# Kernel optimization log

Hardware: AMD Instinct MI355X
Metric: run time of the kernel (lower is better)

## Reference

```python
import jax, jax.numpy as jnp
import numpy as np

B, N, M = 8, 1024, 1024
D_MODEL, D_HEAD, M_BITS = 1024, 128, 32
SCALE = 1.0 / np.sqrt(M_BITS)


def setup_inputs() -> dict:
    key = jax.random.key(0)
    ks = jax.random.split(key, 11)
    w_std = 1.0 / np.sqrt(D_MODEL)  # ~ nn.Linear init scale
    f32 = jnp.float32
    return {
        "Q": jax.random.normal(ks[0], (B, N, D_MODEL), dtype=f32),
        "K": jax.random.normal(ks[1], (B, M, D_MODEL), dtype=f32),
        "V": jax.random.normal(ks[2], (B, M, D_MODEL), dtype=f32),
        "Wq_boolean": jax.random.normal(ks[3], (D_MODEL, M_BITS), dtype=f32) * w_std,
        "Wk_boolean": jax.random.normal(ks[4], (D_MODEL, M_BITS), dtype=f32) * w_std,
        "Wq_tropical": jax.random.normal(ks[5], (D_MODEL, M_BITS), dtype=f32) * w_std,
        "Wk_tropical": jax.random.normal(ks[6], (D_MODEL, M_BITS), dtype=f32) * w_std,
        "Wq_real": jax.random.normal(ks[7], (D_MODEL, M_BITS), dtype=f32) * w_std,
        "Wk_real": jax.random.normal(ks[8], (D_MODEL, M_BITS), dtype=f32) * w_std,
        "Wv": jax.random.normal(ks[9], (D_MODEL, D_HEAD), dtype=f32) * w_std,
        "fusion_weights": jnp.ones((3,), dtype=f32),
        "mask": jnp.ones((B, N, M), dtype=jnp.int32),
    }


def _tropical_sim(Qe, Ke):
    # max-plus (tropical) witness similarity: sim[b,n,m] = max_d (Qe[b,n,d] + Ke[b,m,d])
    # loop over the small fixed bit dim (M_BITS=32) to avoid a [B,N,M,M_BITS] tensor
    acc = Qe[:, :, 0][:, :, None] + Ke[:, :, 0][:, None, :]
    for b in range(1, M_BITS):
        acc = jnp.maximum(acc, Qe[:, :, b][:, :, None] + Ke[:, :, b][:, None, :])
    return acc  # [B,N,M]


def reference(Q, K, V, Wq_boolean, Wk_boolean, Wq_tropical, Wk_tropical,
              Wq_real, Wk_real, Wv, fusion_weights, mask):
    # --- boolean monoid: hard-binarized codes, bit-match count ---
    Qb = (Q @ Wq_boolean > 0).astype(Q.dtype)   # [B,N,m]
    Kb = (K @ Wk_boolean > 0).astype(K.dtype)   # [B,M,m]
    sim_bool = (jnp.einsum('bnd,bmd->bnm', Qb, Kb)
                + jnp.einsum('bnd,bmd->bnm', 1.0 - Qb, 1.0 - Kb))
    # --- tropical monoid: max-plus over continuous codes ---
    sim_trop = _tropical_sim(Q @ Wq_tropical, K @ Wk_tropical)
    # --- real monoid: inner product of continuous codes ---
    sim_real = jnp.einsum('bnd,bmd->bnm', Q @ Wq_real, K @ Wk_real)
    # --- learned fusion + scaled softmax attention ---
    w = jax.nn.softmax(fusion_weights)
    scores = (w[0] * sim_bool + w[1] * sim_trop + w[2] * sim_real) * SCALE
    scores = jnp.where(mask == 0, -jnp.inf, scores)
    attn = jax.nn.softmax(scores, axis=-1)     # [B,N,M]  (dropout: eval mode, identity)
    out = jnp.einsum('bnm,bmh->bnh', attn, V @ Wv)  # [B,N,d_head]
    return out, attn
```

## Files before the change

kernel.cpp:

```cpp
#include <hip/hip_runtime.h>
#include <hip/hip_fp16.h>
#include <stdint.h>
#include <math.h>


#define SCALE_F 0.17677669529663687f

typedef float4 f4;
typedef unsigned int uint_t;
typedef unsigned short ushort_t;
typedef __attribute__((ext_vector_type(8))) short s16x8;
typedef __attribute__((ext_vector_type(8))) unsigned short u16x8;
typedef __attribute__((ext_vector_type(4))) float f32x4;

__device__ __forceinline__ ushort_t f2bf(float x) {
    unsigned u = __float_as_uint(x);
    return (ushort_t)((u + 0x7FFFu + ((u >> 16) & 1u)) >> 16);
}
__device__ __forceinline__ float bf2f(ushort_t h) {
    return __uint_as_float(((unsigned)h) << 16);
}
__device__ __forceinline__ float f4c(const f4 v, int i) {
    return i == 0 ? v.x : (i == 1 ? v.y : (i == 2 ? v.z : v.w));
}
__device__ __forceinline__ unsigned pk_add(unsigned a, unsigned b) {
    unsigned r;
    asm("v_pk_add_f16 %0, %1, %2" : "=v"(r) : "v"(a), "v"(b));
    return r;
}
__device__ __forceinline__ unsigned pk_max(unsigned a, unsigned b) {
    unsigned r;
    asm("v_pk_max_f16 %0, %1, %2" : "=v"(r) : "v"(a), "v"(b));
    return r;
}
__device__ __forceinline__ float h2f(ushort_t u) {
    __half h;
    *reinterpret_cast<ushort_t*>(&h) = u;
    return __half2float(h);
}
__device__ __forceinline__ ushort_t f2h(float x) {
    __half h = __float2half(x);
    return *reinterpret_cast<ushort_t*>(&h);
}

#define MFMA16(a, b, c) __builtin_amdgcn_mfma_f32_16x16x32_bf16((a), (b), (c), 0, 0, 0)

__device__ __forceinline__ int bo(int col, int kq) {
    return col * 64 + 8 * (kq ^ (col & 7));
}
__device__ __forceinline__ int fillk(int s) {
    return 8 * ((s & 7) ^ ((s >> 3) & 7));
}

__global__ __launch_bounds__(256)
void conv_w_kernel(const float* __restrict__ Wqb, const float* __restrict__ Wkb,
                   const float* __restrict__ Wqt, const float* __restrict__ Wkt,
                   const float* __restrict__ Wqr, const float* __restrict__ Wkr,
                   const float* __restrict__ Wv,
                   ushort_t* __restrict__ Wh, ushort_t* __restrict__ Wm,
                   ushort_t* __restrict__ Wl3,
                   ushort_t* __restrict__ Wvh, ushort_t* __restrict__ Wvm) {
    __shared__ float T[256][33];
    const int t = threadIdx.x;
    const int bid = blockIdx.x;
    const float* src;
    int kb, outRowBase, srcStride, srcColBase, side = 0;
    bool isQK, isBool;
    if (bid < 24) {
        side = bid / 12;
        int cb = (bid % 12) / 4;
        kb = bid & 3;
        const float* mats[6] = {Wqb, Wqt, Wqr, Wkb, Wkt, Wkr};
        src = mats[side * 3 + cb];
        srcStride = 32; srcColBase = 0;
        outRowBase = side * 96 + cb * 32;
        isQK = true; isBool = (cb == 0);
    } else {
        int v = bid - 24;
        int hb = v >> 2; kb = v & 3;
        src = Wv; srcStride = 128; srcColBase = hb * 32;
        outRowBase = hb * 32;
        isQK = false; isBool = false;
    }
    #pragma unroll
    for (int i = 0; i < 8; ++i) {
        int idx = t + i * 256;
        int r = idx >> 3, c4 = idx & 7;
        f4 v = *(const f4*)&src[(size_t)(kb * 256 + r) * srcStride + srcColBase + c4 * 4];
        T[r][c4 * 4 + 0] = v.x; T[r][c4 * 4 + 1] = v.y;
        T[r][c4 * 4 + 2] = v.z; T[r][c4 * 4 + 3] = v.w;
    }
    __syncthreads();
    const int col = t >> 3, kseg = t & 7;
    ushort_t* dh = isQK ? Wh : Wvh;
    ushort_t* dm = isQK ? Wm : Wvm;
    size_t obase = (size_t)(outRowBase + col) * 1024 + kb * 256 + kseg * 32;
    u16x8 ph[4], pm[4], pl[4];
    #pragma unroll
    for (int i = 0; i < 32; ++i) {
        float x = T[kseg * 32 + i][col];
        ushort_t hb_ = f2bf(x);
        float r1 = x - bf2f(hb_);
        ushort_t mb_ = f2bf(r1);
        float r2 = r1 - bf2f(mb_);
        ph[i >> 3][i & 7] = hb_;
        pm[i >> 3][i & 7] = mb_;
        pl[i >> 3][i & 7] = f2bf(r2);
    }
    #pragma unroll
    for (int i = 0; i < 4; ++i) {
        *(u16x8*)&dh[obase + i * 8] = ph[i];
        *(u16x8*)&dm[obase + i * 8] = pm[i];
    }
    if (isBool) {
        size_t lbase = (size_t)(side * 32 + col) * 1024 + kb * 256 + kseg * 32;
        #pragma unroll
        for (int i = 0; i < 4; ++i) *(u16x8*)&Wl3[lbase + i * 8] = pl[i];
    }
}


__global__ __launch_bounds__(256)
void proj_qk_kernel(const float* __restrict__ Q, const float* __restrict__ K,
                    const ushort_t* __restrict__ Wh, const ushort_t* __restrict__ Wm,
                    ushort_t* __restrict__ Qt_q, ushort_t* __restrict__ Kt_q,
                    ushort_t* __restrict__ Qrh, ushort_t* __restrict__ Qrm,
                    ushort_t* __restrict__ Krh, ushort_t* __restrict__ Krm,
                    uint_t* __restrict__ Qbits, uint_t* __restrict__ Kbits) {
    __shared__ ushort_t BH[2][6144];
    __shared__ ushort_t BM[2][4096];
    __shared__ uint_t sb[32];
    const int t = threadIdx.x, lane = t & 63, w = t >> 6;
    const int g = lane >> 4, l15 = lane & 15;
    const int side = blockIdx.x >> 8;
    const int tile = blockIdx.x & 255;
    const int row0 = tile * 32;
    const int rg = w >> 1;
    const int ch = w & 1;
    const float* __restrict__ X = side ? K : Q;
    const float* __restrict__ Xrow = X + (size_t)(row0 + rg * 16 + l15) * 1024;
    if (t < 32) sb[t] = 0;

    const ushort_t* srcH[3]; int dstH[3];
    #pragma unroll
    for (int i = 0; i < 3; ++i) {
        int s = t + i * 256;
        int col = s >> 3;
        srcH[i] = Wh + (size_t)(side * 96 + col) * 1024 + fillk(s);
        dstH[i] = s * 8;
    }
    const ushort_t* srcM[2]; int dstM[2];
    #pragma unroll
    for (int i = 0; i < 2; ++i) {
        int s = t + i * 256;
        int col = s >> 3;
        int f = (col < 32) ? col : col + 32;
        srcM[i] = Wm + (size_t)(side * 96 + f) * 1024 + fillk(s);
        dstM[i] = s * 8;
    }

    f32x4 accB[2], accT[2], accR[2];
    #pragma unroll
    for (int i = 0; i < 2; ++i) {
        accB[i] = f32x4{0.f, 0.f, 0.f, 0.f};
        accT[i] = f32x4{0.f, 0.f, 0.f, 0.f};
        accR[i] = f32x4{0.f, 0.f, 0.f, 0.f};
    }

    f4 arE[4], arO[4];
    u16x8 hE[3], mE[2], hO[3], mO[2];

    auto STAGE_A = [&](int k0, f4* ar) {
        ar[0] = *(const f4*)&Xrow[k0 + g * 8];
        ar[1] = *(const f4*)&Xrow[k0 + g * 8 + 4];
        ar[2] = *(const f4*)&Xrow[k0 + 32 + g * 8];
        ar[3] = *(const f4*)&Xrow[k0 + 32 + g * 8 + 4];
    };
    auto STAGE_B = [&](int k0, u16x8* hh, u16x8* mm) {
        #pragma unroll
        for (int i = 0; i < 3; ++i) hh[i] = *(const u16x8*)(srcH[i] + k0);
        #pragma unroll
        for (int i = 0; i < 2; ++i) mm[i] = *(const u16x8*)(srcM[i] + k0);
    };
    auto WRITE_B = [&](int buf, u16x8* hh, u16x8* mm) {
        #pragma unroll
        for (int i = 0; i < 3; ++i) *(u16x8*)&BH[buf][dstH[i]] = hh[i];
        #pragma unroll
        for (int i = 0; i < 2; ++i) *(u16x8*)&BM[buf][dstM[i]] = mm[i];
    };
    auto COMPUTE = [&](int buf, f4* ar) {
        #pragma unroll
        for (int ks = 0; ks < 2; ++ks) {
            u16x8 ah, am, al;
            #pragma unroll
            for (int j = 0; j < 8; ++j) {
                float x = (j < 4) ? f4c(ar[2 * ks], j) : f4c(ar[2 * ks + 1], j - 4);
                ushort_t hb_ = f2bf(x);
                float r1 = x - bf2f(hb_);
                ushort_t mb_ = f2bf(r1);
                ah[j] = hb_; am[j] = mb_;
                al[j] = f2bf(r1 - bf2f(mb_));
            }
            s16x8 a1 = (s16x8)ah, a2 = (s16x8)am;
            const int kq = ks * 4 + g;
            if (ch == 0) {
                s16x8 a3 = (s16x8)al;
                #pragma unroll
                for (int cf = 0; cf < 2; ++cf) {
                    int col = cf * 16 + l15;
                    s16x8 bh = *(const s16x8*)&BH[buf][bo(col, kq)];
                    s16x8 bm = *(const s16x8*)&BM[buf][bo(col, kq)];
                    accB[cf] = MFMA16(a1, bh, accB[cf]);
                    accB[cf] = MFMA16(a1, bm, accB[cf]);
                    accB[cf] = MFMA16(a2, bh, accB[cf]);
                    accB[cf] = MFMA16(a2, bm, accB[cf]);
                    accB[cf] = MFMA16(a3, bh, accB[cf]);
                }
            } else {
                #pragma unroll
                for (int cf = 0; cf < 2; ++cf) {
                    int col = 32 + cf * 16 + l15;
                    s16x8 bh = *(const s16x8*)&BH[buf][bo(col, kq)];
                    accT[cf] = MFMA16(a1, bh, accT[cf]);
                }
                #pragma unroll
                for (int cf = 0; cf < 2; ++cf) {
                    int colh = 64 + cf * 16 + l15;
                    int colm = 32 + cf * 16 + l15;
                    s16x8 bh = *(const s16x8*)&BH[buf][bo(colh, kq)];
                    s16x8 bm = *(const s16x8*)&BM[buf][bo(colm, kq)];
                    accR[cf] = MFMA16(a1, bh, accR[cf]);
                    accR[cf] = MFMA16(a1, bm, accR[cf]);
                    accR[cf] = MFMA16(a2, bh, accR[cf]);
                }
            }
        }
    };

    STAGE_A(0, arE);
    STAGE_B(0, hE, mE);
    WRITE_B(0, hE, mE);
    __syncthreads();
    for (int cc = 0; cc < 8; ++cc) {
        const int kE = cc * 128;
        STAGE_A(kE + 64, arO);
        STAGE_B(kE + 64, hO, mO);
        COMPUTE(0, arE);
        WRITE_B(1, hO, mO);
        __syncthreads();
        if (cc < 7) {
            STAGE_A(kE + 128, arE);
            STAGE_B(kE + 128, hE, mE);
        }
        COMPUTE(1, arO);
        if (cc < 7) WRITE_B(0, hE, mE);
        __syncthreads();
    }

    if (ch == 0) {
        #pragma unroll
        for (int cf = 0; cf < 2; ++cf)
            #pragma unroll
            for (int r = 0; r < 4; ++r) {
                unsigned long long bm = __ballot(accB[cf][r] > 0.f);
                if (lane == 0) {
                    #pragma unroll
                    for (int gg = 0; gg < 4; ++gg)
                        sb[rg * 16 + gg * 4 + r] |=
                            (uint_t)((bm >> (16 * gg)) & 0xFFFFull) << (16 * cf);
                }
            }
    } else {
        ushort_t* Tt = side ? Kt_q : Qt_q;
        ushort_t* Rh = side ? Krh : Qrh;
        ushort_t* Rm = side ? Krm : Qrm;
        #pragma unroll
        for (int cf = 0; cf < 2; ++cf)
            #pragma unroll
            for (int r = 0; r < 4; ++r) {
                int grow = row0 + rg * 16 + g * 4 + r;
                Tt[(size_t)grow * 32 + cf * 16 + l15] = f2h(accT[cf][r]);
                float v = accR[cf][r];
                ushort_t h = f2bf(v);
                Rh[(size_t)grow * 32 + cf * 16 + l15] = h;
                Rm[(size_t)grow * 32 + cf * 16 + l15] = f2bf(v - bf2f(h));
            }
    }
    __syncthreads();
    uint_t* Tb = side ? Kbits : Qbits;
    if (t < 32) Tb[row0 + t] = sb[t];
}


__global__ __launch_bounds__(256)
void proj_v_kernel(const float* __restrict__ V,
                   const ushort_t* __restrict__ Wvh, const ushort_t* __restrict__ Wvm,
                   ushort_t* __restrict__ VphT, ushort_t* __restrict__ VpmT) {
    __shared__ ushort_t VH[2][8192], VM[2][8192];
    const int t = threadIdx.x, lane = t & 63, w = t >> 6;
    const int g = lane >> 4, l15 = lane & 15;
    const int tile = blockIdx.x;
    const int row0 = tile * 16;
    const int hbase = w * 32;
    const float* __restrict__ Xrow = V + (size_t)(row0 + l15) * 1024;

    const ushort_t* srcH[4]; const ushort_t* srcM[4]; int dst[4];
    #pragma unroll
    for (int i = 0; i < 4; ++i) {
        int s = t + i * 256;
        int col = s >> 3;
        srcH[i] = Wvh + (size_t)col * 1024 + fillk(s);
        srcM[i] = Wvm + (size_t)col * 1024 + fillk(s);
        dst[i] = s * 8;
    }

    f32x4 acc[2];
    acc[0] = f32x4{0.f, 0.f, 0.f, 0.f};
    acc[1] = f32x4{0.f, 0.f, 0.f, 0.f};

    f4 arE[4], arO[4];
    u16x8 hE[4], mE[4], hO[4], mO[4];

    auto STAGE_A = [&](int k0, f4* ar) {
        ar[0] = *(const f4*)&Xrow[k0 + g * 8];
        ar[1] = *(const f4*)&Xrow[k0 + g * 8 + 4];
        ar[2] = *(const f4*)&Xrow[k0 + 32 + g * 8];
        ar[3] = *(const f4*)&Xrow[k0 + 32 + g * 8 + 4];
    };
    auto STAGE_B = [&](int k0, u16x8* hh, u16x8* mm) {
        #pragma unroll
        for (int i = 0; i < 4; ++i) {
            hh[i] = *(const u16x8*)(srcH[i] + k0);
            mm[i] = *(const u16x8*)(srcM[i] + k0);
        }
    };
    auto WRITE_B = [&](int buf, u16x8* hh, u16x8* mm) {
        #pragma unroll
        for (int i = 0; i < 4; ++i) {
            *(u16x8*)&VH[buf][dst[i]] = hh[i];
            *(u16x8*)&VM[buf][dst[i]] = mm[i];
        }
    };
    auto COMPUTE = [&](int buf, f4* ar) {
        #pragma unroll
        for (int ks = 0; ks < 2; ++ks) {
            u16x8 ah, am;
            #pragma unroll
            for (int j = 0; j < 8; ++j) {
                float x = (j < 4) ? f4c(ar[2 * ks], j) : f4c(ar[2 * ks + 1], j - 4);
                ushort_t hb_ = f2bf(x);
                ah[j] = hb_; am[j] = f2bf(x - bf2f(hb_));
            }
            s16x8 a1 = (s16x8)ah, a2 = (s16x8)am;
            const int kq = ks * 4 + g;
            #pragma unroll
            for (int cf = 0; cf < 2; ++cf) {
                int col = hbase + cf * 16 + l15;
                s16x8 bh = *(const s16x8*)&VH[buf][bo(col, kq)];
                s16x8 bm = *(const s16x8*)&VM[buf][bo(col, kq)];
                acc[cf] = MFMA16(a1, bh, acc[cf]);
                acc[cf] = MFMA16(a1, bm, acc[cf]);
                acc[cf] = MFMA16(a2, bh, acc[cf]);
            }
        }
    };

    STAGE_A(0, arE);
    STAGE_B(0, hE, mE);
    WRITE_B(0, hE, mE);
    __syncthreads();
    for (int cc = 0; cc < 8; ++cc) {
        const int kE = cc * 128;
        STAGE_A(kE + 64, arO);
        STAGE_B(kE + 64, hO, mO);
        COMPUTE(0, arE);
        WRITE_B(1, hO, mO);
        __syncthreads();
        if (cc < 7) {
            STAGE_A(kE + 128, arE);
            STAGE_B(kE + 128, hE, mE);
        }
        COMPUTE(1, arO);
        if (cc < 7) WRITE_B(0, hE, mE);
        __syncthreads();
    }

    const int b = tile >> 6;
    const int mb = (tile & 63) * 16 + g * 4;
    #pragma unroll
    for (int cf = 0; cf < 2; ++cf) {
        int colh = hbase + cf * 16 + l15;
        float v0 = acc[cf][0], v1 = acc[cf][1], v2 = acc[cf][2], v3 = acc[cf][3];
        ushort_t h0 = f2bf(v0), h1 = f2bf(v1), h2_ = f2bf(v2), h3 = f2bf(v3);
        ushort4 hv = make_ushort4(h0, h1, h2_, h3);
        ushort4 mv = make_ushort4(f2bf(v0 - bf2f(h0)), f2bf(v1 - bf2f(h1)),
                                  f2bf(v2 - bf2f(h2_)), f2bf(v3 - bf2f(h3)));
        size_t ob = (size_t)(b * 128 + colh) * 1024 + mb;
        *(ushort4*)&VphT[ob] = hv;
        *(ushort4*)&VpmT[ob] = mv;
    }
}


#define SW 1036

__global__ __launch_bounds__(256)
void fused_attn_kernel(const ushort_t* __restrict__ Qt_q, const ushort_t* __restrict__ Kt_q,
                       const ushort_t* __restrict__ Qrh, const ushort_t* __restrict__ Qrm,
                       const ushort_t* __restrict__ Krh, const ushort_t* __restrict__ Krm,
                       const uint_t* __restrict__ Qbits, const uint_t* __restrict__ Kbits,
                       const ushort_t* __restrict__ VphT, const ushort_t* __restrict__ VpmT,
                       const int* __restrict__ mask, const float* __restrict__ fw,
                       float* __restrict__ attn, float* __restrict__ out) {
    __shared__ uint_t S[16][SW];
    __shared__ float rmaxS[16], rinvS[16];
    const int t = threadIdx.x, lane = t & 63, w = t >> 6;
    const int g = lane >> 4, l15 = lane & 15;
    const int bid = blockIdx.x;
    const int b = bid & 7, n0 = (bid >> 3) * 16;
    const int rowA = b * 1024 + n0;

    s16x8 qrh = *(const s16x8*)&Qrh[(size_t)(rowA + l15) * 32 + g * 8];
    s16x8 qrm = *(const s16x8*)&Qrm[(size_t)(rowA + l15) * 32 + g * 8];
    uint_t qt[4][16], qb[4];
    #pragma unroll
    for (int r = 0; r < 4; ++r) {
        const uint_t* p = (const uint_t*)&Qt_q[(size_t)(rowA + 4 * g + r) * 32];
        #pragma unroll
        for (int j = 0; j < 16; ++j) qt[r][j] = p[j];
        qb[r] = Qbits[rowA + 4 * g + r];
    }
    const float f0 = fw[0], f1 = fw[1], f2 = fw[2];
    const float fm = fmaxf(f0, fmaxf(f1, f2));
    const float e0 = __expf(f0 - fm), e1 = __expf(f1 - fm), e2 = __expf(f2 - fm);
    const float wi = 1.f / (e0 + e1 + e2);
    const float w0 = e0 * wi, w1 = e1 * wi, w2 = e2 * wi;

    for (int i = 0; i < 16; ++i) {
        const int m0 = (w + 4 * i) * 16;
        const int mrow = b * 1024 + m0;
        const uint_t* ktp = (const uint_t*)&Kt_q[(size_t)(mrow + l15) * 32];
        uint_t kk[16];
        uint4 k0v = *(const uint4*)&ktp[0];
        uint4 k1v = *(const uint4*)&ktp[4];
        uint4 k2v = *(const uint4*)&ktp[8];
        uint4 k3v = *(const uint4*)&ktp[12];
        kk[0] = k0v.x; kk[1] = k0v.y; kk[2] = k0v.z; kk[3] = k0v.w;
        kk[4] = k1v.x; kk[5] = k1v.y; kk[6] = k1v.z; kk[7] = k1v.w;
        kk[8] = k2v.x; kk[9] = k2v.y; kk[10] = k2v.z; kk[11] = k2v.w;
        kk[12] = k3v.x; kk[13] = k3v.y; kk[14] = k3v.z; kk[15] = k3v.w;
        s16x8 krh = *(const s16x8*)&Krh[(size_t)(mrow + l15) * 32 + g * 8];
        s16x8 krm = *(const s16x8*)&Krm[(size_t)(mrow + l15) * 32 + g * 8];
        uint_t kb = Kbits[mrow + l15];
        int mk[4];
        #pragma unroll
        for (int r = 0; r < 4; ++r)
            mk[r] = mask[(size_t)(rowA + 4 * g + r) * 1024 + m0 + l15];

        f32x4 rc = f32x4{0.f, 0.f, 0.f, 0.f};
        rc = MFMA16(qrh, krh, rc);
        rc = MFMA16(qrh, krm, rc);
        rc = MFMA16(qrm, krh, rc);

        float trop[4];
        #pragma unroll
        for (int r = 0; r < 4; ++r) {
            unsigned a = pk_add(qt[r][0], kk[0]);
            #pragma unroll
            for (int j = 1; j < 16; ++j)
                a = pk_max(a, pk_add(qt[r][j], kk[j]));
            trop[r] = fmaxf(h2f((ushort_t)(a & 0xFFFF)), h2f((ushort_t)(a >> 16)));
        }
        #pragma unroll
        for (int r = 0; r < 4; ++r) {
            float cnt = (float)(32 - __popc(qb[r] ^ kb));
            float s = (w0 * cnt + w1 * trop[r] + w2 * rc[r]) * SCALE_F;
            *(float*)&S[4 * g + r][m0 + l15] = mk[r] ? s : -INFINITY;
        }
    }
    __syncthreads();

    #pragma unroll
    for (int q = 0; q < 4; ++q) {
        const int row = 4 * w + q;
        float mx = -INFINITY;
        #pragma unroll
        for (int j = 0; j < 16; ++j)
            mx = fmaxf(mx, *(const float*)&S[row][lane + j * 64]);
        #pragma unroll
        for (int off = 32; off >= 1; off >>= 1) mx = fmaxf(mx, __shfl_xor(mx, off, 64));
        float sm = 0.f;
        #pragma unroll
        for (int j = 0; j < 16; ++j)
            sm += __expf(*(const float*)&S[row][lane + j * 64] - mx);
        #pragma unroll
        for (int off = 32; off >= 1; off >>= 1) sm += __shfl_xor(sm, off, 64);
        if (lane == 0) { rmaxS[row] = mx; rinvS[row] = 1.f / sm; }
    }
    __syncthreads();

    #pragma unroll
    for (int j = 0; j < 16; ++j) {
        const float mx = rmaxS[j], inv = rinvS[j];
        f4 s4 = *(const f4*)&S[j][t * 4];
        float p0 = __expf(s4.x - mx) * inv;
        float p1 = __expf(s4.y - mx) * inv;
        float p2 = __expf(s4.z - mx) * inv;
        float p3 = __expf(s4.w - mx) * inv;
        *(f4*)&attn[(size_t)(rowA + j) * 1024 + t * 4] = make_float4(p0, p1, p2, p3);
        ushort_t h0 = f2bf(p0), h1 = f2bf(p1), h2_ = f2bf(p2), h3 = f2bf(p3);
        uint4 pk;
        pk.x = (uint_t)h0 | ((uint_t)f2bf(p0 - bf2f(h0)) << 16);
        pk.y = (uint_t)h1 | ((uint_t)f2bf(p1 - bf2f(h1)) << 16);
        pk.z = (uint_t)h2_ | ((uint_t)f2bf(p2 - bf2f(h2_)) << 16);
        pk.w = (uint_t)h3 | ((uint_t)f2bf(p3 - bf2f(h3)) << 16);
        *(uint4*)&S[j][t * 4] = pk;
    }
    __syncthreads();

    const int hbase = w * 32;
    f32x4 acc[2];
    acc[0] = f32x4{0.f, 0.f, 0.f, 0.f};
    acc[1] = f32x4{0.f, 0.f, 0.f, 0.f};
    for (int mc = 0; mc < 32; ++mc) {
        const int m0 = mc * 32;
        uint4 ua = *(const uint4*)&S[l15][m0 + g * 8];
        uint4 ub = *(const uint4*)&S[l15][m0 + g * 8 + 4];
        u16x8 a1v, a2v;
        uint_t uu[8] = {ua.x, ua.y, ua.z, ua.w, ub.x, ub.y, ub.z, ub.w};
        #pragma unroll
        for (int j = 0; j < 8; ++j) {
            a1v[j] = (ushort_t)(uu[j] & 0xFFFFu);
            a2v[j] = (ushort_t)(uu[j] >> 16);
        }
        s16x8 a1 = (s16x8)a1v, a2 = (s16x8)a2v;
        #pragma unroll
        for (int cf = 0; cf < 2; ++cf) {
            const size_t vb = (size_t)(b * 128 + hbase + cf * 16 + l15) * 1024 + m0 + g * 8;
            s16x8 bh = *(const s16x8*)&VphT[vb];
            s16x8 bm = *(const s16x8*)&VpmT[vb];
            acc[cf] = MFMA16(a1, bh, acc[cf]);
            acc[cf] = MFMA16(a1, bm, acc[cf]);
            acc[cf] = MFMA16(a2, bh, acc[cf]);
        }
    }
    #pragma unroll
    for (int cf = 0; cf < 2; ++cf)
        #pragma unroll
        for (int r = 0; r < 4; ++r)
            out[(size_t)(rowA + 4 * g + r) * 128 + hbase + cf * 16 + l15] = acc[cf][r];
}


extern "C" void kernel_launch(void* const* d_in, const int* in_sizes, int n_in,
                              void* d_out, int out_size, void* d_ws, size_t ws_size,
                              hipStream_t stream) {
    const float* Q   = (const float*)d_in[0];
    const float* K   = (const float*)d_in[1];
    const float* V   = (const float*)d_in[2];
    const float* Wqb = (const float*)d_in[3];
    const float* Wkb = (const float*)d_in[4];
    const float* Wqt = (const float*)d_in[5];
    const float* Wkt = (const float*)d_in[6];
    const float* Wqr = (const float*)d_in[7];
    const float* Wkr = (const float*)d_in[8];
    const float* Wv  = (const float*)d_in[9];
    const float* fw  = (const float*)d_in[10];
    const int*  mask = (const int*)d_in[11];

    ushort_t* wsu = (ushort_t*)d_ws;
    ushort_t* Wh   = wsu;
    ushort_t* Wm   = Wh + 196608;
    ushort_t* Wl3  = Wm + 196608;
    ushort_t* Wvh  = Wl3 + 65536;
    ushort_t* Wvm  = Wvh + 131072;
    ushort_t* Qt_q = Wvm + 131072;
    ushort_t* Kt_q = Qt_q + 262144;
    ushort_t* Qrh  = Kt_q + 262144;
    ushort_t* Qrm  = Qrh + 262144;
    ushort_t* Krh  = Qrm + 262144;
    ushort_t* Krm  = Krh + 262144;
    ushort_t* VphT = Krm + 262144;
    ushort_t* VpmT = VphT + 1048576;
    uint_t* Qbits = (uint_t*)(VpmT + 1048576);
    uint_t* Kbits = Qbits + 8192;

    float* out  = (float*)d_out;
    float* attn = out + 1048576;

    conv_w_kernel<<<40, 256, 0, stream>>>(Wqb, Wkb, Wqt, Wkt, Wqr, Wkr, Wv,
                                          Wh, Wm, Wl3, Wvh, Wvm);
    proj_qk_kernel<<<512, 256, 0, stream>>>(Q, K, Wh, Wm,
                                            Qt_q, Kt_q, Qrh, Qrm, Krh, Krm, Qbits, Kbits);
    proj_v_kernel<<<512, 256, 0, stream>>>(V, Wvh, Wvm, VphT, VpmT);
    fused_attn_kernel<<<512, 256, 0, stream>>>(Qt_q, Kt_q, Qrh, Qrm, Krh, Krm,
                                               Qbits, Kbits, VphT, VpmT,
                                               mask, fw, attn, out);
}
```

Measured before the change: 267.8 us.

## Halve rows per block in projection kernels to double grid and occupancy

New measurement: 362.8 us. 1.35x slower.

```diff
diff --git a/kernel.cpp b/kernel.cpp
--- a/kernel.cpp
+++ b/kernel.cpp
@@ -120,26 +120,25 @@
 }
 
 
-__global__ __launch_bounds__(256)
+__global__ __launch_bounds__(256, 4)
 void proj_qk_kernel(const float* __restrict__ Q, const float* __restrict__ K,
                     const ushort_t* __restrict__ Wh, const ushort_t* __restrict__ Wm,
                     ushort_t* __restrict__ Qt_q, ushort_t* __restrict__ Kt_q,
                     ushort_t* __restrict__ Qrh, ushort_t* __restrict__ Qrm,
                     ushort_t* __restrict__ Krh, ushort_t* __restrict__ Krm,
                     uint_t* __restrict__ Qbits, uint_t* __restrict__ Kbits) {
-    __shared__ ushort_t BH[2][6144];
-    __shared__ ushort_t BM[2][4096];
-    __shared__ uint_t sb[32];
+    __shared__ ushort_t POOL[20480];
+    ushort_t* BH = POOL;
+    ushort_t* BM = POOL + 12288;
     const int t = threadIdx.x, lane = t & 63, w = t >> 6;
     const int g = lane >> 4, l15 = lane & 15;
-    const int side = blockIdx.x >> 8;
-    const int tile = blockIdx.x & 255;
-    const int row0 = tile * 32;
-    const int rg = w >> 1;
-    const int ch = w & 1;
+    const int side = blockIdx.x >> 9;
+    const int tile = blockIdx.x & 511;
+    const int row0 = tile * 16;
+    const bool isBool = (w < 2);
+    const int cf = w & 1;
     const float* __restrict__ X = side ? K : Q;
-    const float* __restrict__ Xrow = X + (size_t)(row0 + rg * 16 + l15) * 1024;
-    if (t < 32) sb[t] = 0;
+    const float* __restrict__ Xrow = X + (size_t)(row0 + l15) * 1024;
 
     const ushort_t* srcH[3]; int dstH[3];
     #pragma unroll
@@ -159,13 +158,8 @@
         dstM[i] = s * 8;
     }
 
-    f32x4 accB[2], accT[2], accR[2];
-    #pragma unroll
-    for (int i = 0; i < 2; ++i) {
-        accB[i] = f32x4{0.f, 0.f, 0.f, 0.f};
-        accT[i] = f32x4{0.f, 0.f, 0.f, 0.f};
-        accR[i] = f32x4{0.f, 0.f, 0.f, 0.f};
-    }
+    f32x4 accA = f32x4{0.f, 0.f, 0.f, 0.f};
+    f32x4 accC = f32x4{0.f, 0.f, 0.f, 0.f};
 
     f4 arE[4], arO[4];
     u16x8 hE[3], mE[2], hO[3], mO[2];
@@ -184,9 +178,9 @@
     };
     auto WRITE_B = [&](int buf, u16x8* hh, u16x8* mm) {
         #pragma unroll
-        for (int i = 0; i < 3; ++i) *(u16x8*)&BH[buf][dstH[i]] = hh[i];
-        #pragma unroll
-        for (int i = 0; i < 2; ++i) *(u16x8*)&BM[buf][dstM[i]] = mm[i];
+        for (int i = 0; i < 3; ++i) *(u16x8*)&BH[buf * 6144 + dstH[i]] = hh[i];
+        #pragma unroll
+        for (int i = 0; i < 2; ++i) *(u16x8*)&BM[buf * 4096 + dstM[i]] = mm[i];
     };
     auto COMPUTE = [&](int buf, f4* ar) {
         #pragma unroll
@@ -203,36 +197,27 @@
             }
             s16x8 a1 = (s16x8)ah, a2 = (s16x8)am;
             const int kq = ks * 4 + g;
-            if (ch == 0) {
+            if (isBool) {
                 s16x8 a3 = (s16x8)al;
-                #pragma unroll
-                for (int cf = 0; cf < 2; ++cf) {
-                    int col = cf * 16 + l15;
-                    s16x8 bh = *(const s16x8*)&BH[buf][bo(col, kq)];
-                    s16x8 bm = *(const s16x8*)&BM[buf][bo(col, kq)];
-                    accB[cf] = MFMA16(a1, bh, accB[cf]);
-                    accB[cf] = MFMA16(a1, bm, accB[cf]);
-                    accB[cf] = MFMA16(a2, bh, accB[cf]);
-                    accB[cf] = MFMA16(a2, bm, accB[cf]);
-                    accB[cf] = MFMA16(a3, bh, accB[cf]);
-                }
+                int col = cf * 16 + l15;
+                s16x8 bh = *(const s16x8*)&BH[buf * 6144 + bo(col, kq)];
+                s16x8 bm = *(const s16x8*)&BM[buf * 4096 + bo(col, kq)];
+                accA = MFMA16(a1, bh, accA);
+                accA = MFMA16(a1, bm, accA);
+                accA = MFMA16(a2, bh, accA);
+                accA = MFMA16(a2, bm, accA);
+                accA = MFMA16(a3, bh, accA);
             } else {
-                #pragma unroll
-                for (int cf = 0; cf < 2; ++cf) {
-                    int col = 32 + cf * 16 + l15;
-                    s16x8 bh = *(const s16x8*)&BH[buf][bo(col, kq)];
-                    accT[cf] = MFMA16(a1, bh, accT[cf]);
-                }
-                #pragma unroll
-                for (int cf = 0; cf < 2; ++cf) {
-                    int colh = 64 + cf * 16 + l15;
-                    int colm = 32 + cf * 16 + l15;
-                    s16x8 bh = *(const s16x8*)&BH[buf][bo(colh, kq)];
-                    s16x8 bm = *(const s16x8*)&BM[buf][bo(colm, kq)];
-                    accR[cf] = MFMA16(a1, bh, accR[cf]);
-                    accR[cf] = MFMA16(a1, bm, accR[cf]);
-                    accR[cf] = MFMA16(a2, bh, accR[cf]);
-                }
+                int colT = 32 + cf * 16 + l15;
+                s16x8 bhT = *(const s16x8*)&BH[buf * 6144 + bo(colT, kq)];
+                accA = MFMA16(a1, bhT, accA);
+                int colh = 64 + cf * 16 + l15;
+                int colm = 32 + cf * 16 + l15;
+                s16x8 bh = *(const s16x8*)&BH[buf * 6144 + bo(colh, kq)];
+                s16x8 bm = *(const s16x8*)&BM[buf * 4096 + bo(colm, kq)];
+                accC = MFMA16(a1, bh, accC);
+                accC = MFMA16(a1, bm, accC);
+                accC = MFMA16(a2, bh, accC);
             }
         }
     };
@@ -257,147 +242,141 @@
         __syncthreads();
     }
 
-    if (ch == 0) {
-        #pragma unroll
-        for (int cf = 0; cf < 2; ++cf)
-            #pragma unroll
-            for (int r = 0; r < 4; ++r) {
-                unsigned long long bm = __ballot(accB[cf][r] > 0.f);
-                if (lane == 0) {
-                    #pragma unroll
-                    for (int gg = 0; gg < 4; ++gg)
-                        sb[rg * 16 + gg * 4 + r] |=
-                            (uint_t)((bm >> (16 * gg)) & 0xFFFFull) << (16 * cf);
-                }
+    uint_t* sbp = (uint_t*)POOL;
+    if (t < 32) sbp[t] = 0;
+    __syncthreads();
+    if (isBool) {
+        #pragma unroll
+        for (int r = 0; r < 4; ++r) {
+            unsigned long long bm = __ballot(accA[r] > 0.f);
+            if (lane == 0) {
+                #pragma unroll
+                for (int gg = 0; gg < 4; ++gg)
+                    sbp[cf * 16 + gg * 4 + r] =
+                        (uint_t)((bm >> (16 * gg)) & 0xFFFFull) << (16 * cf);
             }
+        }
     } else {
         ushort_t* Tt = side ? Kt_q : Qt_q;
         ushort_t* Rh = side ? Krh : Qrh;
         ushort_t* Rm = side ? Krm : Qrm;
         #pragma unroll
-        for (int cf = 0; cf < 2; ++cf)
-            #pragma unroll
-            for (int r = 0; r < 4; ++r) {
-                int grow = row0 + rg * 16 + g * 4 + r;
-                Tt[(size_t)grow * 32 + cf * 16 + l15] = f2h(accT[cf][r]);
-                float v = accR[cf][r];
-                ushort_t h = f2bf(v);
-                Rh[(size_t)grow * 32 + cf * 16 + l15] = h;
-                Rm[(size_t)grow * 32 + cf * 16 + l15] = f2bf(v - bf2f(h));
-            }
+        for (int r = 0; r < 4; ++r) {
+            int grow = row0 + 4 * g + r;
+            Tt[(size_t)grow * 32 + cf * 16 + l15] = f2h(accA[r]);
+            float v = accC[r];
+            ushort_t h = f2bf(v);
+            Rh[(size_t)grow * 32 + cf * 16 + l15] = h;
+            Rm[(size_t)grow * 32 + cf * 16 + l15] = f2bf(v - bf2f(h));
+        }
     }
     __syncthreads();
     uint_t* Tb = side ? Kbits : Qbits;
-    if (t < 32) Tb[row0 + t] = sb[t];
-}
-
-
-__global__ __launch_bounds__(256)
+    if (t < 16) Tb[row0 + t] = sbp[t] | sbp[16 + t];
+}
+
+
+__global__ __launch_bounds__(256, 4)
 void proj_v_kernel(const float* __restrict__ V,
                    const ushort_t* __restrict__ Wvh, const ushort_t* __restrict__ Wvm,
                    ushort_t* __restrict__ VphT, ushort_t* __restrict__ VpmT) {
-    __shared__ ushort_t VH[2][8192], VM[2][8192];
+    __shared__ ushort_t PL[2][8192];
     const int t = threadIdx.x, lane = t & 63, w = t >> 6;
     const int g = lane >> 4, l15 = lane & 15;
     const int tile = blockIdx.x;
-    const int row0 = tile * 16;
+    const int row0 = tile * 8;
     const int hbase = w * 32;
-    const float* __restrict__ Xrow = V + (size_t)(row0 + l15) * 1024;
-
-    const ushort_t* srcH[4]; const ushort_t* srcM[4]; int dst[4];
+    const float* __restrict__ Xrow = V + (size_t)(row0 + (l15 & 7)) * 1024;
+
+    const ushort_t* srcV[4]; int dstV[4];
     #pragma unroll
     for (int i = 0; i < 4; ++i) {
         int s = t + i * 256;
-        int col = s >> 3;
-        srcH[i] = Wvh + (size_t)col * 1024 + fillk(s);
-        srcM[i] = Wvm + (size_t)col * 1024 + fillk(s);
-        dst[i] = s * 8;
+        int c = s >> 3, p8 = s & 7;
+        int hp = p8 >> 2, q = p8 & 3;
+        int lvl = hp ^ (c & 1);
+        int kq = q ^ ((c >> 1) & 3);
+        srcV[i] = (lvl ? Wvm : Wvh) + (size_t)c * 1024 + kq * 8;
+        dstV[i] = s * 8;
     }
 
     f32x4 acc[2];
     acc[0] = f32x4{0.f, 0.f, 0.f, 0.f};
     acc[1] = f32x4{0.f, 0.f, 0.f, 0.f};
 
-    f4 arE[4], arO[4];
-    u16x8 hE[4], mE[4], hO[4], mO[4];
+    f4 arE[2], arO[2];
+    u16x8 vE[4], vO[4];
 
     auto STAGE_A = [&](int k0, f4* ar) {
         ar[0] = *(const f4*)&Xrow[k0 + g * 8];
         ar[1] = *(const f4*)&Xrow[k0 + g * 8 + 4];
-        ar[2] = *(const f4*)&Xrow[k0 + 32 + g * 8];
-        ar[3] = *(const f4*)&Xrow[k0 + 32 + g * 8 + 4];
-    };
-    auto STAGE_B = [&](int k0, u16x8* hh, u16x8* mm) {
-        #pragma unroll
-        for (int i = 0; i < 4; ++i) {
-            hh[i] = *(const u16x8*)(srcH[i] + k0);
-            mm[i] = *(const u16x8*)(srcM[i] + k0);
-        }
-    };
-    auto WRITE_B = [&](int buf, u16x8* hh, u16x8* mm) {
-        #pragma unroll
-        for (int i = 0; i < 4; ++i) {
-            *(u16x8*)&VH[buf][dst[i]] = hh[i];
-            *(u16x8*)&VM[buf][dst[i]] = mm[i];
-        }
+    };
+    auto STAGE_B = [&](int k0, u16x8* vv) {
+        #pragma unroll
+        for (int i = 0; i < 4; ++i) vv[i] = *(const u16x8*)(srcV[i] + k0);
+    };
+    auto WRITE_B = [&](int buf, u16x8* vv) {
+        #pragma unroll
+        for (int i = 0; i < 4; ++i) *(u16x8*)&PL[buf][dstV[i]] = vv[i];
     };
     auto COMPUTE = [&](int buf, f4* ar) {
-        #pragma unroll
-        for (int ks = 0; ks < 2; ++ks) {
-            u16x8 ah, am;
-            #pragma unroll
-            for (int j = 0; j < 8; ++j) {
-                float x = (j < 4) ? f4c(ar[2 * ks], j) : f4c(ar[2 * ks + 1], j - 4);
-                ushort_t hb_ = f2bf(x);
-                ah[j] = hb_; am[j] = f2bf(x - bf2f(hb_));
-            }
-            s16x8 a1 = (s16x8)ah, a2 = (s16x8)am;
-            const int kq = ks * 4 + g;
-            #pragma unroll
-            for (int cf = 0; cf < 2; ++cf) {
-                int col = hbase + cf * 16 + l15;
-                s16x8 bh = *(const s16x8*)&VH[buf][bo(col, kq)];
-                s16x8 bm = *(const s16x8*)&VM[buf][bo(col, kq)];
-                acc[cf] = MFMA16(a1, bh, acc[cf]);
-                acc[cf] = MFMA16(a1, bm, acc[cf]);
-                acc[cf] = MFMA16(a2, bh, acc[cf]);
-            }
+        u16x8 ah, am;
+        #pragma unroll
+        for (int j = 0; j < 8; ++j) {
+            float x = (j < 4) ? f4c(ar[0], j) : f4c(ar[1], j - 4);
+            ushort_t hb_ = f2bf(x);
+            ah[j] = hb_; am[j] = f2bf(x - bf2f(hb_));
+        }
+        s16x8 a1 = (s16x8)ah, a2 = (s16x8)am;
+        #pragma unroll
+        for (int cfi = 0; cfi < 2; ++cfi) {
+            int c = hbase + cfi * 16 + l15;
+            int sw = 8 * (g ^ ((c >> 1) & 3));
+            int aH = c * 64 + ((0 ^ (c & 1)) * 32) + sw;
+            int aM = c * 64 + ((1 ^ (c & 1)) * 32) + sw;
+            s16x8 bh = *(const s16x8*)&PL[buf][aH];
+            s16x8 bm = *(const s16x8*)&PL[buf][aM];
+            acc[cfi] = MFMA16(a1, bh, acc[cfi]);
+            acc[cfi] = MFMA16(a1, bm, acc[cfi]);
+            acc[cfi] = MFMA16(a2, bh, acc[cfi]);
         }
     };
 
     STAGE_A(0, arE);
-    STAGE_B(0, hE, mE);
-    WRITE_B(0, hE, mE);
-    __syncthreads();
-    for (int cc = 0; cc < 8; ++cc) {
-        const int kE = cc * 128;
-        STAGE_A(kE + 64, arO);
-        STAGE_B(kE + 64, hO, mO);
+    STAGE_B(0, vE);
+    WRITE_B(0, vE);
+    __syncthreads();
+    for (int cc2 = 0; cc2 < 16; ++cc2) {
+        const int k = cc2 * 64;
+        STAGE_A(k + 32, arO);
+        STAGE_B(k + 32, vO);
         COMPUTE(0, arE);
-        WRITE_B(1, hO, mO);
+        WRITE_B(1, vO);
         __syncthreads();
-        if (cc < 7) {
-            STAGE_A(kE + 128, arE);
-            STAGE_B(kE + 128, hE, mE);
+        if (cc2 < 15) {
+            STAGE_A(k + 64, arE);
+            STAGE_B(k + 64, vE);
         }
         COMPUTE(1, arO);
-        if (cc < 7) WRITE_B(0, hE, mE);
+        if (cc2 < 15) WRITE_B(0, vE);
         __syncthreads();
     }
 
-    const int b = tile >> 6;
-    const int mb = (tile & 63) * 16 + g * 4;
-    #pragma unroll
-    for (int cf = 0; cf < 2; ++cf) {
-        int colh = hbase + cf * 16 + l15;
-        float v0 = acc[cf][0], v1 = acc[cf][1], v2 = acc[cf][2], v3 = acc[cf][3];
-        ushort_t h0 = f2bf(v0), h1 = f2bf(v1), h2_ = f2bf(v2), h3 = f2bf(v3);
-        ushort4 hv = make_ushort4(h0, h1, h2_, h3);
-        ushort4 mv = make_ushort4(f2bf(v0 - bf2f(h0)), f2bf(v1 - bf2f(h1)),
-                                  f2bf(v2 - bf2f(h2_)), f2bf(v3 - bf2f(h3)));
-        size_t ob = (size_t)(b * 128 + colh) * 1024 + mb;
-        *(ushort4*)&VphT[ob] = hv;
-        *(ushort4*)&VpmT[ob] = mv;
+    if (g < 2) {
+        const int b = tile >> 7;
+        const int mb = (tile & 127) * 8 + 4 * g;
+        #pragma unroll
+        for (int cfi = 0; cfi < 2; ++cfi) {
+            int colh = hbase + cfi * 16 + l15;
+            float v0 = acc[cfi][0], v1 = acc[cfi][1], v2 = acc[cfi][2], v3 = acc[cfi][3];
+            ushort_t h0 = f2bf(v0), h1 = f2bf(v1), h2_ = f2bf(v2), h3 = f2bf(v3);
+            ushort4 hv = make_ushort4(h0, h1, h2_, h3);
+            ushort4 mv = make_ushort4(f2bf(v0 - bf2f(h0)), f2bf(v1 - bf2f(h1)),
+                                      f2bf(v2 - bf2f(h2_)), f2bf(v3 - bf2f(h3)));
+            size_t ob = (size_t)(b * 128 + colh) * 1024 + mb;
+            *(ushort4*)&VphT[ob] = hv;
+            *(ushort4*)&VpmT[ob] = mv;
+        }
     }
 }
 
@@ -535,20 +514,20 @@
         }
         s16x8 a1 = (s16x8)a1v, a2 = (s16x8)a2v;
         #pragma unroll
-        for (int cf = 0; cf < 2; ++cf) {
-            const size_t vb = (size_t)(b * 128 + hbase + cf * 16 + l15) * 1024 + m0 + g * 8;
+        for (int cfi = 0; cfi < 2; ++cfi) {
+            const size_t vb = (size_t)(b * 128 + hbase + cfi * 16 + l15) * 1024 + m0 + g * 8;
             s16x8 bh = *(const s16x8*)&VphT[vb];
             s16x8 bm = *(const s16x8*)&VpmT[vb];
-            acc[cf] = MFMA16(a1, bh, acc[cf]);
-            acc[cf] = MFMA16(a1, bm, acc[cf]);
-            acc[cf] = MFMA16(a2, bh, acc[cf]);
-        }
-    }
-    #pragma unroll
-    for (int cf = 0; cf < 2; ++cf)
+            acc[cfi] = MFMA16(a1, bh, acc[cfi]);
+            acc[cfi] = MFMA16(a1, bm, acc[cfi]);
+            acc[cfi] = MFMA16(a2, bh, acc[cfi]);
+        }
+    }
+    #pragma unroll
+    for (int cfi = 0; cfi < 2; ++cfi)
         #pragma unroll
         for (int r = 0; r < 4; ++r)
-            out[(size_t)(rowA + 4 * g + r) * 128 + hbase + cf * 16 + l15] = acc[cf][r];
+            out[(size_t)(rowA + 4 * g + r) * 128 + hbase + cfi * 16 + l15] = acc[cfi][r];
 }
 
 
@@ -590,9 +569,9 @@
 
     conv_w_kernel<<<40, 256, 0, stream>>>(Wqb, Wkb, Wqt, Wkt, Wqr, Wkr, Wv,
                                           Wh, Wm, Wl3, Wvh, Wvm);
-    proj_qk_kernel<<<512, 256, 0, stream>>>(Q, K, Wh, Wm,
-                                            Qt_q, Kt_q, Qrh, Qrm, Krh, Krm, Qbits, Kbits);
-    proj_v_kernel<<<512, 256, 0, stream>>>(V, Wvh, Wvm, VphT, VpmT);
+    proj_qk_kernel<<<1024, 256, 0, stream>>>(Q, K, Wh, Wm,
+                                             Qt_q, Kt_q, Qrh, Qrm, Krh, Krm, Qbits, Kbits);
+    proj_v_kernel<<<1024, 256, 0, stream>>>(V, Wvh, Wvm, VphT, VpmT);
     fused_attn_kernel<<<512, 256, 0, stream>>>(Qt_q, Kt_q, Qrh, Qrm, Krh, Krm,
                                                Qbits, Kbits, VphT, VpmT,
                                                mask, fw, attn, out);
```
